# Performance work log

Hardware: AMD Instinct MI355X
Metric: run time of the kernel (lower is better)

## Reference

```python
import jax, jax.numpy as jnp
import numpy as np

SIZE = (128, 128, 128)


def _base_grid():
    # (3, D, H, W): channel i holds the index along spatial dim i (ij meshgrid)
    vs = [jnp.arange(s, dtype=jnp.float32) for s in SIZE]
    return jnp.stack(jnp.meshgrid(*vs, indexing='ij'))


def _grid_sample_3d(vol, grid):
    """torch.nn.functional.grid_sample 3D, mode='bilinear' (trilinear),
    padding_mode='border', align_corners=True.
    vol: (B, C, D, H, W); grid: (B, D, H, W, 3) with last dim = (x, y, z)
    mapping to (W, H, D) axes, per torch semantics."""
    B, C, D, H, W = vol.shape
    gx, gy, gz = grid[..., 0], grid[..., 1], grid[..., 2]
    # unnormalize (align_corners=True) and clamp (border padding)
    ix = jnp.clip((gx + 1.0) * 0.5 * (W - 1), 0.0, W - 1)
    iy = jnp.clip((gy + 1.0) * 0.5 * (H - 1), 0.0, H - 1)
    iz = jnp.clip((gz + 1.0) * 0.5 * (D - 1), 0.0, D - 1)
    ix0f, iy0f, iz0f = jnp.floor(ix), jnp.floor(iy), jnp.floor(iz)
    wx, wy, wz = ix - ix0f, iy - iy0f, iz - iz0f  # (B, D, H, W)
    ix0 = ix0f.astype(jnp.int32)
    iy0 = iy0f.astype(jnp.int32)
    iz0 = iz0f.astype(jnp.int32)
    ix1 = jnp.minimum(ix0 + 1, W - 1)
    iy1 = jnp.minimum(iy0 + 1, H - 1)
    iz1 = jnp.minimum(iz0 + 1, D - 1)

    def sample_one(v, z0, z1, y0, y1, x0, x1, wz_, wy_, wx_):
        # v: (C, D, H, W); index arrays: (D, H, W)
        def g(z, y, x):
            return v[:, z, y, x]  # (C, D, H, W)
        wz_, wy_, wx_ = wz_[None], wy_[None], wx_[None]  # broadcast over C
        c000 = g(z0, y0, x0); c001 = g(z0, y0, x1)
        c010 = g(z0, y1, x0); c011 = g(z0, y1, x1)
        c100 = g(z1, y0, x0); c101 = g(z1, y0, x1)
        c110 = g(z1, y1, x0); c111 = g(z1, y1, x1)
        c00 = c000 * (1 - wx_) + c001 * wx_
        c01 = c010 * (1 - wx_) + c011 * wx_
        c10 = c100 * (1 - wx_) + c101 * wx_
        c11 = c110 * (1 - wx_) + c111 * wx_
        c0 = c00 * (1 - wy_) + c01 * wy_
        c1 = c10 * (1 - wy_) + c11 * wy_
        return c0 * (1 - wz_) + c1 * wz_

    return jax.vmap(sample_one)(vol, iz0, iz1, iy0, iy1, ix0, ix1, wz, wy, wx)


def _warp_dvf(dvf_to_warp, dvf_to_apply):
    g = _base_grid()[None] + dvf_to_apply  # (B, 3, D, H, W)
    scale = jnp.array([2.0 / (s - 1) for s in SIZE], dtype=jnp.float32).reshape(1, 3, 1, 1, 1)
    g = g * scale - 1.0  # 2*(g/(size-1) - 0.5)
    g = jnp.transpose(g, (0, 2, 3, 4, 1))  # (B, D, H, W, 3)
    return _grid_sample_3d(dvf_to_warp, g)


def setup_inputs() -> dict:
    key = jax.random.key(0)
    k1, k2 = jax.random.split(key)
    B = 2
    shape = (B, 3) + SIZE
    return {
        'dvf_fwd': jax.random.normal(k1, shape, dtype=jnp.float32),
        'dvf_bwd': jax.random.normal(k2, shape, dtype=jnp.float32),
    }


def reference(dvf_fwd, dvf_bwd):
    dvf_bwd_warped = _warp_dvf(dvf_bwd, dvf_fwd)
    cycle_error_fwd = dvf_fwd + dvf_bwd_warped
    dvf_fwd_warped = _warp_dvf(dvf_fwd, dvf_bwd)
    cycle_error_bwd = dvf_bwd + dvf_fwd_warped
    return jnp.mean(cycle_error_fwd ** 2) + jnp.mean(cycle_error_bwd ** 2)
```

## Files before the change

kernel.cpp:

```cpp
#include <hip/hip_runtime.h>


#define CS    2097152
#define BS    (3*CS)
#define NTHR  256
#define NBLK_MAIN 8192
#define INV_N (1.0f/12582912.0f)

#if defined(__has_builtin)
#if __has_builtin(__builtin_amdgcn_cvt_pk_fp8_f32) && __has_builtin(__builtin_amdgcn_cvt_pk_f32_fp8)
#define HW_FP8 1
#endif
#endif

typedef float v2f __attribute__((ext_vector_type(2)));
struct __attribute__((aligned(8))) U4 { unsigned x, y, z, w; };

__device__ __forceinline__ unsigned enc1_sw(float x) {
    union { float f; unsigned u; } v; v.f = x;
    unsigned s = v.u >> 31;
    float ax = fminf(fabsf(x), 448.0f);
    if (ax < 0.015625f) return s << 7;
    v.f = ax;
    unsigned u = v.u;
    u += 0x7FFFF + ((u >> 20) & 1);
    unsigned e = (u >> 23) - 120;
    if (e > 15) { e = 15; u = 0x7u << 20; }
    return (s << 7) | (e << 3) | ((u >> 20) & 7);
}
__device__ __forceinline__ float dec1_sw(unsigned b) {
    unsigned s = b >> 7, e = (b >> 3) & 15, m = b & 7;
    union { unsigned u; float f; } v;
    if (e == 0) { float r = (float)m * 0.001953125f; return s ? -r : r; }
    v.u = (s << 31) | ((e + 120) << 23) | (m << 20);
    return v.f;
}
template <bool HI>
__device__ __forceinline__ unsigned enc_pk(float a, float b, unsigned old) {
#ifdef HW_FP8
    return (unsigned)__builtin_amdgcn_cvt_pk_fp8_f32(a, b, (int)old, HI);
#else
    unsigned p = enc1_sw(a) | (enc1_sw(b) << 8);
    return HI ? ((old & 0x0000FFFFu) | (p << 16)) : ((old & 0xFFFF0000u) | p);
#endif
}
template <bool HI>
__device__ __forceinline__ v2f dec_pk(unsigned u) {
#ifdef HW_FP8
    return __builtin_amdgcn_cvt_pk_f32_fp8((int)u, HI);
#else
    unsigned p = HI ? (u >> 16) : u;
    v2f r; r.x = dec1_sw(p & 255); r.y = dec1_sw((p >> 8) & 255);
    return r;
#endif
}
__device__ __forceinline__ uint2 enc_entry(float c0, float c1, float c2,
                                           float p0, float p1, float p2) {
    unsigned lo = enc_pk<false>(c0, c1, 0);
    lo = enc_pk<true>(c2, p0, lo);
    unsigned hi = enc_pk<false>(p1, p2, 0);
    return make_uint2(lo, hi);
}

__global__ __launch_bounds__(NTHR)
void repack_fp8(const float* __restrict__ F, const float* __restrict__ G,
                uint2* __restrict__ PF, uint2* __restrict__ PG) {
    unsigned g = blockIdx.x * NTHR + threadIdx.x;
    int field = g >> 20;
    int b = (g >> 19) & 1;
    unsigned q = g & 0x7FFFF;
    int x = (q & 31) << 2;
    int y = (q >> 5) & 127;
    int z = q >> 12;
    int y1 = min(y + 1, 127);
    const float* src = (field ? G : F) + b * BS;
    uint2* dst = (field ? PG : PF) + b * CS;
    int i0 = (z << 14) + (y << 7) + x;
    int i1 = (z << 14) + (y1 << 7) + x;
    float4 A  = *(const float4*)(src + i0);
    float4 Bc = *(const float4*)(src + CS + i0);
    float4 Cc = *(const float4*)(src + 2 * CS + i0);
    float4 Ap = *(const float4*)(src + i1);
    float4 Bp = *(const float4*)(src + CS + i1);
    float4 Cp = *(const float4*)(src + 2 * CS + i1);
    uint2 e0 = enc_entry(A.x, Bc.x, Cc.x, Ap.x, Bp.x, Cp.x);
    uint2 e1 = enc_entry(A.y, Bc.y, Cc.y, Ap.y, Bp.y, Cp.y);
    uint2 e2 = enc_entry(A.z, Bc.z, Cc.z, Ap.z, Bp.z, Cp.z);
    uint2 e3 = enc_entry(A.w, Bc.w, Cc.w, Ap.w, Bp.w, Cp.w);
    U4 o0; o0.x = e0.x; o0.y = e0.y; o0.z = e1.x; o0.w = e1.y;
    U4 o1; o1.x = e2.x; o1.y = e2.y; o1.z = e3.x; o1.w = e3.y;
    *(U4*)(dst + i0) = o0;
    *(U4*)(dst + i0 + 2) = o1;
}

__global__ __launch_bounds__(NTHR, 8)
void icl_main(const uint2* __restrict__ PF, const uint2* __restrict__ PG,
              const float* __restrict__ F, const float* __restrict__ G,
              float* __restrict__ partial) {
    __shared__ float sA[3072];

    int orig = blockIdx.x;
    int xcd = orig & 7;
    int s = orig >> 3;
    int u = s & 63, tile = s >> 6;
    int ht = ((tile & 7) << 3) | (u & 7);
    int wt = ((tile >> 3) << 3) | (u >> 3);
    int dt = xcd & 1, b = (xcd >> 1) & 1, dir = xcd >> 2;

    const float* Ab = (dir ? G : F) + b * BS;
    const uint2* Vb = (dir ? PF : PG) + b * CS;
    int d0 = dt << 6, h0 = ht << 1, w0 = wt << 3;

    int t = threadIdx.x;
    #pragma unroll
    for (int j = 0; j < 3; ++j) {
        int rem = t << 2;
        int d_l = rem >> 4, h_l = (rem >> 3) & 1, w_l = rem & 7;
        const float4 v = *(const float4*)(Ab + j * CS + ((d0 + d_l) << 14)
                                          + ((h0 + h_l) << 7) + w0 + w_l);
        int Rb = (j * 2 + h_l) * 8 + w_l;
        sA[((Rb + 0) << 6) | ((d_l + Rb + 0) & 63)] = v.x;
        sA[((Rb + 1) << 6) | ((d_l + Rb + 1) & 63)] = v.y;
        sA[((Rb + 2) << 6) | ((d_l + Rb + 2) & 63)] = v.z;
        sA[((Rb + 3) << 6) | ((d_l + Rb + 3) & 63)] = v.w;
    }
    __syncthreads();

    int lane = t & 63, wv = t >> 6;
    int h_l = wv & 1, wseg = wv >> 1;
    int d = d0 + lane, h = h0 + h_l;

    float A0[4], A1[4], A2[4], WX[4], WY[4], WZ[4];
    int AD0[4], AD1[4];
    #pragma unroll
    for (int i = 0; i < 4; ++i) {
        int w_l = (wseg << 2) | i;
        int w = w0 + w_l;
        int R0 = h_l * 8 + w_l, R1 = 16 + R0, R2 = 32 + R0;
        float a0 = sA[(R0 << 6) | ((lane + R0) & 63)];
        float a1 = sA[(R1 << 6) | ((lane + R1) & 63)];
        float a2 = sA[(R2 << 6) | ((lane + R2) & 63)];
        float fx = fminf(fmaxf((float)d + a0, 0.0f), 127.0f);
        float fy = fminf(fmaxf((float)h + a1, 0.0f), 127.0f);
        float fz = fminf(fmaxf((float)w + a2, 0.0f), 127.0f);
        int x0 = (int)fx, y0 = (int)fy, z0 = (int)fz;
        int x0c = min(x0, 126);
        int z1 = min(z0 + 1, 127);
        A0[i] = a0; A1[i] = a1; A2[i] = a2;
        WX[i] = fx - (float)x0c;
        WY[i] = fy - (float)y0;
        WZ[i] = fz - (float)z0;
        AD0[i] = (((z0 << 7) | y0) << 7) + x0c;
        AD1[i] = (((z1 << 7) | y0) << 7) + x0c;
    }
    U4 QA[4], QB[4];
    #pragma unroll
    for (int i = 0; i < 4; ++i) QA[i] = *(const U4*)(Vb + AD0[i]);
    #pragma unroll
    for (int i = 0; i < 4; ++i) QB[i] = *(const U4*)(Vb + AD1[i]);

    float acc = 0.0f;
    #pragma unroll
    for (int i = 0; i < 4; ++i) {
        float wxp = WX[i], wy = WY[i], wz = WZ[i];
        U4 qa = QA[i], qb = QB[i];
        v2f a_lo = dec_pk<false>(qa.x), b_lo = dec_pk<false>(qa.z);
        v2f c_lo = dec_pk<false>(qb.x), d_lo = dec_pk<false>(qb.z);
        float t0 = a_lo.x + wxp * (b_lo.x - a_lo.x);
        float t1 = a_lo.y + wxp * (b_lo.y - a_lo.y);
        float s0 = c_lo.x + wxp * (d_lo.x - c_lo.x);
        float s1 = c_lo.y + wxp * (d_lo.y - c_lo.y);
        float u0 = t0 + wz * (s0 - t0);
        float u1 = t1 + wz * (s1 - t1);
        v2f a_hi = dec_pk<true>(qa.x), b_hi = dec_pk<true>(qa.z);
        v2f c_hi = dec_pk<true>(qb.x), d_hi = dec_pk<true>(qb.z);
        float t2 = a_hi.x + wxp * (b_hi.x - a_hi.x);
        float t3 = a_hi.y + wxp * (b_hi.y - a_hi.y);
        float s2 = c_hi.x + wxp * (d_hi.x - c_hi.x);
        float s3 = c_hi.y + wxp * (d_hi.y - c_hi.y);
        float u2 = t2 + wz * (s2 - t2);
        float u3 = t3 + wz * (s3 - t3);
        v2f a2_ = dec_pk<false>(qa.y), b2_ = dec_pk<false>(qa.w);
        v2f c2_ = dec_pk<false>(qb.y), d2_ = dec_pk<false>(qb.w);
        float t4 = a2_.x + wxp * (b2_.x - a2_.x);
        float t5 = a2_.y + wxp * (b2_.y - a2_.y);
        float s4 = c2_.x + wxp * (d2_.x - c2_.x);
        float s5 = c2_.y + wxp * (d2_.y - c2_.y);
        float u4 = t4 + wz * (s4 - t4);
        float u5 = t5 + wz * (s5 - t5);
        float e0 = A0[i] + (u0 + wy * (u3 - u0));
        float e1 = A1[i] + (u1 + wy * (u4 - u1));
        float e2 = A2[i] + (u2 + wy * (u5 - u2));
        acc += e0 * e0 + e1 * e1 + e2 * e2;
    }

    #pragma unroll
    for (int o = 32; o > 0; o >>= 1) acc += __shfl_down(acc, o);
    __shared__ float ws[NTHR / 64];
    if ((t & 63) == 0) ws[t >> 6] = acc;
    __syncthreads();
    if (t == 0) {
        float ssum = 0.0f;
        #pragma unroll
        for (int i = 0; i < NTHR / 64; ++i) ssum += ws[i];
        partial[orig] = ssum;
    }
}

__device__ __forceinline__ float tri_fb(const float* __restrict__ v,
                                        int zy00, int zy01, int zy10, int zy11,
                                        int x0, int x1,
                                        float wz, float wy, float wx) {
    float c000 = v[zy00 + x0], c001 = v[zy00 + x1];
    float c010 = v[zy01 + x0], c011 = v[zy01 + x1];
    float c100 = v[zy10 + x0], c101 = v[zy10 + x1];
    float c110 = v[zy11 + x0], c111 = v[zy11 + x1];
    float c00 = c000 + wx * (c001 - c000);
    float c01 = c010 + wx * (c011 - c010);
    float c10 = c100 + wx * (c101 - c100);
    float c11 = c110 + wx * (c111 - c110);
    float c0  = c00  + wy * (c01  - c00);
    float c1  = c10  + wy * (c11  - c10);
    return c0 + wz * (c1 - c0);
}

__global__ __launch_bounds__(NTHR, 6)
void icl_partial_fb(const float* __restrict__ F, const float* __restrict__ G,
                    float* __restrict__ partial) {
    __shared__ float sA[6144];
    int orig = blockIdx.x;
    int id = ((orig & 7) << 9) | (orig >> 3);
    int wt  = id & 15;
    int ht  = (id >> 4) & 31;
    int dt  = (id >> 9) & 1;
    int b   = (id >> 10) & 1;
    int dir = id >> 11;
    const float* Ab = (dir ? G : F) + b * BS;
    const float* Vb = (dir ? F : G) + b * BS;
    int d0 = dt << 6, h0 = ht << 2, w0 = wt << 3;
    int t = threadIdx.x;
    #pragma unroll
    for (int j = 0; j < 6; ++j) {
        int L   = (j << 10) + (t << 2);
        int c   = L >> 11;
        int rem = L & 2047;
        int row = rem >> 3;
        int w_l = rem & 7;
        int d_l = row >> 2, h_l = row & 3;
        const float4 v = *(const float4*)(Ab + c * CS + ((d0 + d_l) << 14)
                                          + ((h0 + h_l) << 7) + w0 + w_l);
        int Rb = (c * 4 + h_l) * 8 + w_l;
        sA[((Rb + 0) << 6) | ((d_l + Rb + 0) & 63)] = v.x;
        sA[((Rb + 1) << 6) | ((d_l + Rb + 1) & 63)] = v.y;
        sA[((Rb + 2) << 6) | ((d_l + Rb + 2) & 63)] = v.z;
        sA[((Rb + 3) << 6) | ((d_l + Rb + 3) & 63)] = v.w;
    }
    __syncthreads();
    int lane = t & 63, wv = t >> 6;
    int d = d0 + lane;
    float acc = 0.0f;
    #pragma unroll 4
    for (int i = 0; i < 8; ++i) {
        int h = h0 + wv, w = w0 + i;
        int R0 = (0 * 4 + wv) * 8 + i;
        int R1 = (1 * 4 + wv) * 8 + i;
        int R2 = (2 * 4 + wv) * 8 + i;
        float a0 = sA[(R0 << 6) | ((lane + R0) & 63)];
        float a1 = sA[(R1 << 6) | ((lane + R1) & 63)];
        float a2 = sA[(R2 << 6) | ((lane + R2) & 63)];
        float fx = fminf(fmaxf((float)d + a0, 0.0f), 127.0f);
        float fy = fminf(fmaxf((float)h + a1, 0.0f), 127.0f);
        float fz = fminf(fmaxf((float)w + a2, 0.0f), 127.0f);
        int x0 = (int)fx, y0 = (int)fy, z0 = (int)fz;
        float wx = fx - (float)x0, wy = fy - (float)y0, wz = fz - (float)z0;
        int x1 = min(x0 + 1, 127), y1 = min(y0 + 1, 127), z1 = min(z0 + 1, 127);
        int zy00 = ((z0 << 7) | y0) << 7;
        int zy01 = ((z0 << 7) | y1) << 7;
        int zy10 = ((z1 << 7) | y0) << 7;
        int zy11 = ((z1 << 7) | y1) << 7;
        float s0 = tri_fb(Vb,        zy00, zy01, zy10, zy11, x0, x1, wz, wy, wx);
        float s1 = tri_fb(Vb + CS,   zy00, zy01, zy10, zy11, x0, x1, wz, wy, wx);
        float s2 = tri_fb(Vb + 2*CS, zy00, zy01, zy10, zy11, x0, x1, wz, wy, wx);
        float e0 = a0 + s0, e1 = a1 + s1, e2 = a2 + s2;
        acc += e0 * e0 + e1 * e1 + e2 * e2;
    }
    #pragma unroll
    for (int o = 32; o > 0; o >>= 1) acc += __shfl_down(acc, o);
    __shared__ float ws[NTHR / 64];
    if ((t & 63) == 0) ws[t >> 6] = acc;
    __syncthreads();
    if (t == 0) {
        float s = 0.0f;
        #pragma unroll
        for (int i = 0; i < NTHR / 64; ++i) s += ws[i];
        partial[orig] = s;
    }
}

__global__ __launch_bounds__(NTHR)
void icl_final(const float* __restrict__ partial, float* __restrict__ out, int n) {
    float a = 0.0f;
    for (int i = threadIdx.x; i < n; i += NTHR) a += partial[i];
    #pragma unroll
    for (int o = 32; o > 0; o >>= 1) a += __shfl_down(a, o);
    __shared__ float ws[NTHR / 64];
    if ((threadIdx.x & 63) == 0) ws[threadIdx.x >> 6] = a;
    __syncthreads();
    if (threadIdx.x == 0) {
        float s = 0.0f;
        #pragma unroll
        for (int i = 0; i < NTHR / 64; ++i) s += ws[i];
        out[0] = s * INV_N;
    }
}

extern "C" void kernel_launch(void* const* d_in, const int* in_sizes, int n_in,
                              void* d_out, int out_size, void* d_ws, size_t ws_size,
                              hipStream_t stream) {
    const float* F = (const float*)d_in[0];
    const float* G = (const float*)d_in[1];
    size_t field_bytes = (size_t)2 * CS * sizeof(uint2);
    size_t need = 2 * field_bytes + NBLK_MAIN * sizeof(float) + 256;
    if (ws_size >= need) {
        uint2* PF = (uint2*)d_ws;
        uint2* PG = PF + (size_t)2 * CS;
        float* partial = (float*)(PG + (size_t)2 * CS);
        repack_fp8<<<8192, NTHR, 0, stream>>>(F, G, PF, PG);
        icl_main<<<NBLK_MAIN, NTHR, 0, stream>>>(PF, PG, F, G, partial);
        icl_final<<<1, NTHR, 0, stream>>>(partial, (float*)d_out, NBLK_MAIN);
    } else {
        float* partial = (float*)d_ws;
        icl_partial_fb<<<4096, NTHR, 0, stream>>>(F, G, partial);
        icl_final<<<1, NTHR, 0, stream>>>(partial, (float*)d_out, 4096);
    }
}
```

Measured before the change: 88.08 us.

## Pack full 2x2 y/z corner stencil per voxel into 12-byte fp8 entries

```diff
diff --git a/kernel.cpp b/kernel.cpp
--- a/kernel.cpp
+++ b/kernel.cpp
@@ -5,6 +5,7 @@
 #define BS    (3*CS)
 #define NTHR  256
 #define NBLK_MAIN 8192
+#define EB    12
 #define INV_N (1.0f/12582912.0f)
 
 #if defined(__has_builtin)
@@ -14,7 +15,8 @@
 #endif
 
 typedef float v2f __attribute__((ext_vector_type(2)));
-struct __attribute__((aligned(8))) U4 { unsigned x, y, z, w; };
+struct __attribute__((aligned(4))) U4a4 { unsigned x, y, z, w; };
+struct __attribute__((aligned(4))) U2a4 { unsigned x, y; };
 
 __device__ __forceinline__ unsigned enc1_sw(float x) {
     union { float f; unsigned u; } v; v.f = x;
@@ -54,47 +56,60 @@
     return r;
 #endif
 }
-__device__ __forceinline__ uint2 enc_entry(float c0, float c1, float c2,
-                                           float p0, float p1, float p2) {
-    unsigned lo = enc_pk<false>(c0, c1, 0);
-    lo = enc_pk<true>(c2, p0, lo);
-    unsigned hi = enc_pk<false>(p1, p2, 0);
-    return make_uint2(lo, hi);
-}
 
 __global__ __launch_bounds__(NTHR)
-void repack_fp8(const float* __restrict__ F, const float* __restrict__ G,
-                uint2* __restrict__ PF, uint2* __restrict__ PG) {
+void repack_zp(const float* __restrict__ F, const float* __restrict__ G,
+               char* __restrict__ P) {
     unsigned g = blockIdx.x * NTHR + threadIdx.x;
-    int field = g >> 20;
-    int b = (g >> 19) & 1;
-    unsigned q = g & 0x7FFFF;
-    int x = (q & 31) << 2;
-    int y = (q >> 5) & 127;
-    int z = q >> 12;
-    int y1 = min(y + 1, 127);
+    int x = (g & 31) << 2;
+    unsigned r = g >> 5;
+    int y = r & 127;
+    int z = (r >> 7) & 127;
+    int b = (r >> 14) & 1;
+    int field = (r >> 15) & 1;
     const float* src = (field ? G : F) + b * BS;
-    uint2* dst = (field ? PG : PF) + b * CS;
-    int i0 = (z << 14) + (y << 7) + x;
-    int i1 = (z << 14) + (y1 << 7) + x;
-    float4 A  = *(const float4*)(src + i0);
-    float4 Bc = *(const float4*)(src + CS + i0);
-    float4 Cc = *(const float4*)(src + 2 * CS + i0);
-    float4 Ap = *(const float4*)(src + i1);
-    float4 Bp = *(const float4*)(src + CS + i1);
-    float4 Cp = *(const float4*)(src + 2 * CS + i1);
-    uint2 e0 = enc_entry(A.x, Bc.x, Cc.x, Ap.x, Bp.x, Cp.x);
-    uint2 e1 = enc_entry(A.y, Bc.y, Cc.y, Ap.y, Bp.y, Cp.y);
-    uint2 e2 = enc_entry(A.z, Bc.z, Cc.z, Ap.z, Bp.z, Cp.z);
-    uint2 e3 = enc_entry(A.w, Bc.w, Cc.w, Ap.w, Bp.w, Cp.w);
-    U4 o0; o0.x = e0.x; o0.y = e0.y; o0.z = e1.x; o0.w = e1.y;
-    U4 o1; o1.x = e2.x; o1.y = e2.y; o1.z = e3.x; o1.w = e3.y;
-    *(U4*)(dst + i0) = o0;
-    *(U4*)(dst + i0 + 2) = o1;
+    char* dst = P + (size_t)(field * 2 + b) * ((size_t)EB * CS)
+                  + (size_t)((z << 14) + (y << 7) + x) * EB;
+    int y1 = min(y + 1, 127), z1 = min(z + 1, 127);
+    int iA = (z << 14) + (y << 7) + x;
+    int iB = (z << 14) + (y1 << 7) + x;
+    int iC = (z1 << 14) + (y << 7) + x;
+    int iD = (z1 << 14) + (y1 << 7) + x;
+    float4 A0 = *(const float4*)(src + iA);
+    float4 A1 = *(const float4*)(src + CS + iA);
+    float4 A2 = *(const float4*)(src + 2 * CS + iA);
+    float4 B0 = *(const float4*)(src + iB);
+    float4 B1 = *(const float4*)(src + CS + iB);
+    float4 B2 = *(const float4*)(src + 2 * CS + iB);
+    float4 C0 = *(const float4*)(src + iC);
+    float4 C1 = *(const float4*)(src + CS + iC);
+    float4 C2 = *(const float4*)(src + 2 * CS + iC);
+    float4 D0 = *(const float4*)(src + iD);
+    float4 D1 = *(const float4*)(src + CS + iD);
+    float4 D2 = *(const float4*)(src + 2 * CS + iD);
+    const float* pA0 = (const float*)&A0; const float* pA1 = (const float*)&A1;
+    const float* pA2 = (const float*)&A2; const float* pB0 = (const float*)&B0;
+    const float* pB1 = (const float*)&B1; const float* pB2 = (const float*)&B2;
+    const float* pC0 = (const float*)&C0; const float* pC1 = (const float*)&C1;
+    const float* pC2 = (const float*)&C2; const float* pD0 = (const float*)&D0;
+    const float* pD1 = (const float*)&D1; const float* pD2 = (const float*)&D2;
+    unsigned wrd[12];
+    #pragma unroll
+    for (int k = 0; k < 4; ++k) {
+        wrd[3 * k + 0] = enc_pk<true>(pA2[k], pB0[k], enc_pk<false>(pA0[k], pA1[k], 0));
+        wrd[3 * k + 1] = enc_pk<true>(pC0[k], pC1[k], enc_pk<false>(pB1[k], pB2[k], 0));
+        wrd[3 * k + 2] = enc_pk<true>(pD1[k], pD2[k], enc_pk<false>(pC2[k], pD0[k], 0));
+    }
+    U4a4 s0; s0.x = wrd[0]; s0.y = wrd[1]; s0.z = wrd[2]; s0.w = wrd[3];
+    U4a4 s1; s1.x = wrd[4]; s1.y = wrd[5]; s1.z = wrd[6]; s1.w = wrd[7];
+    U4a4 s2; s2.x = wrd[8]; s2.y = wrd[9]; s2.z = wrd[10]; s2.w = wrd[11];
+    *(U4a4*)(dst) = s0;
+    *(U4a4*)(dst + 16) = s1;
+    *(U4a4*)(dst + 32) = s2;
 }
 
 __global__ __launch_bounds__(NTHR, 8)
-void icl_main(const uint2* __restrict__ PF, const uint2* __restrict__ PG,
+void icl_main(const char* __restrict__ P,
               const float* __restrict__ F, const float* __restrict__ G,
               float* __restrict__ partial) {
     __shared__ float sA[3072];
@@ -108,7 +123,7 @@
     int dt = xcd & 1, b = (xcd >> 1) & 1, dir = xcd >> 2;
 
     const float* Ab = (dir ? G : F) + b * BS;
-    const uint2* Vb = (dir ? PF : PG) + b * CS;
+    const char* Vbc = P + (size_t)((dir ? 0 : 2) + b) * ((size_t)EB * CS);
     int d0 = dt << 6, h0 = ht << 1, w0 = wt << 3;
 
     int t = threadIdx.x;
@@ -131,7 +146,7 @@
     int d = d0 + lane, h = h0 + h_l;
 
     float A0[4], A1[4], A2[4], WX[4], WY[4], WZ[4];
-    int AD0[4], AD1[4];
+    int OFF[4];
     #pragma unroll
     for (int i = 0; i < 4; ++i) {
         int w_l = (wseg << 2) | i;
@@ -145,52 +160,43 @@
         float fz = fminf(fmaxf((float)w + a2, 0.0f), 127.0f);
         int x0 = (int)fx, y0 = (int)fy, z0 = (int)fz;
         int x0c = min(x0, 126);
-        int z1 = min(z0 + 1, 127);
         A0[i] = a0; A1[i] = a1; A2[i] = a2;
         WX[i] = fx - (float)x0c;
         WY[i] = fy - (float)y0;
         WZ[i] = fz - (float)z0;
-        AD0[i] = (((z0 << 7) | y0) << 7) + x0c;
-        AD1[i] = (((z1 << 7) | y0) << 7) + x0c;
-    }
-    U4 QA[4], QB[4];
-    #pragma unroll
-    for (int i = 0; i < 4; ++i) QA[i] = *(const U4*)(Vb + AD0[i]);
-    #pragma unroll
-    for (int i = 0; i < 4; ++i) QB[i] = *(const U4*)(Vb + AD1[i]);
+        OFF[i] = ((((z0 << 7) | y0) << 7) + x0c) * EB;
+    }
+    U4a4 QA[4]; U2a4 QB[4];
+    #pragma unroll
+    for (int i = 0; i < 4; ++i) {
+        QA[i] = *(const U4a4*)(Vbc + OFF[i]);
+        QB[i] = *(const U2a4*)(Vbc + OFF[i] + 16);
+    }
 
     float acc = 0.0f;
     #pragma unroll
     for (int i = 0; i < 4; ++i) {
-        float wxp = WX[i], wy = WY[i], wz = WZ[i];
-        U4 qa = QA[i], qb = QB[i];
-        v2f a_lo = dec_pk<false>(qa.x), b_lo = dec_pk<false>(qa.z);
-        v2f c_lo = dec_pk<false>(qb.x), d_lo = dec_pk<false>(qb.z);
-        float t0 = a_lo.x + wxp * (b_lo.x - a_lo.x);
-        float t1 = a_lo.y + wxp * (b_lo.y - a_lo.y);
-        float s0 = c_lo.x + wxp * (d_lo.x - c_lo.x);
-        float s1 = c_lo.y + wxp * (d_lo.y - c_lo.y);
-        float u0 = t0 + wz * (s0 - t0);
-        float u1 = t1 + wz * (s1 - t1);
-        v2f a_hi = dec_pk<true>(qa.x), b_hi = dec_pk<true>(qa.z);
-        v2f c_hi = dec_pk<true>(qb.x), d_hi = dec_pk<true>(qb.z);
-        float t2 = a_hi.x + wxp * (b_hi.x - a_hi.x);
-        float t3 = a_hi.y + wxp * (b_hi.y - a_hi.y);
-        float s2 = c_hi.x + wxp * (d_hi.x - c_hi.x);
-        float s3 = c_hi.y + wxp * (d_hi.y - c_hi.y);
-        float u2 = t2 + wz * (s2 - t2);
-        float u3 = t3 + wz * (s3 - t3);
-        v2f a2_ = dec_pk<false>(qa.y), b2_ = dec_pk<false>(qa.w);
-        v2f c2_ = dec_pk<false>(qb.y), d2_ = dec_pk<false>(qb.w);
-        float t4 = a2_.x + wxp * (b2_.x - a2_.x);
-        float t5 = a2_.y + wxp * (b2_.y - a2_.y);
-        float s4 = c2_.x + wxp * (d2_.x - c2_.x);
-        float s5 = c2_.y + wxp * (d2_.y - c2_.y);
-        float u4 = t4 + wz * (s4 - t4);
-        float u5 = t5 + wz * (s5 - t5);
-        float e0 = A0[i] + (u0 + wy * (u3 - u0));
-        float e1 = A1[i] + (u1 + wy * (u4 - u1));
-        float e2 = A2[i] + (u2 + wy * (u5 - u2));
+        v2f wx2; wx2.x = WX[i]; wx2.y = WX[i];
+        v2f wz2; wz2.x = WZ[i]; wz2.y = WZ[i];
+        float wy = WY[i];
+        v2f p0 = dec_pk<false>(QA[i].x), p1 = dec_pk<true>(QA[i].x);
+        v2f p2 = dec_pk<false>(QA[i].y), p3 = dec_pk<true>(QA[i].y);
+        v2f p4 = dec_pk<false>(QA[i].z), p5 = dec_pk<true>(QA[i].z);
+        v2f q0 = dec_pk<false>(QA[i].w), q1 = dec_pk<true>(QA[i].w);
+        v2f q2 = dec_pk<false>(QB[i].x), q3 = dec_pk<true>(QB[i].x);
+        v2f q4 = dec_pk<false>(QB[i].y), q5 = dec_pk<true>(QB[i].y);
+        v2f X0 = p0 + wx2 * (q0 - p0);
+        v2f X1 = p1 + wx2 * (q1 - p1);
+        v2f X2 = p2 + wx2 * (q2 - p2);
+        v2f X3 = p3 + wx2 * (q3 - p3);
+        v2f X4 = p4 + wx2 * (q4 - p4);
+        v2f X5 = p5 + wx2 * (q5 - p5);
+        v2f Z0 = X0 + wz2 * (X3 - X0);
+        v2f Z1 = X1 + wz2 * (X4 - X1);
+        v2f Z2 = X2 + wz2 * (X5 - X2);
+        float e0 = A0[i] + (Z0.x + wy * (Z1.y - Z0.x));
+        float e1 = A1[i] + (Z0.y + wy * (Z2.x - Z0.y));
+        float e2 = A2[i] + (Z1.x + wy * (Z2.y - Z1.x));
         acc += e0 * e0 + e1 * e1 + e2 * e2;
     }
 
@@ -319,14 +325,13 @@
                               hipStream_t stream) {
     const float* F = (const float*)d_in[0];
     const float* G = (const float*)d_in[1];
-    size_t field_bytes = (size_t)2 * CS * sizeof(uint2);
-    size_t need = 2 * field_bytes + NBLK_MAIN * sizeof(float) + 256;
+    size_t packed_bytes = (size_t)4 * EB * CS;
+    size_t need = packed_bytes + NBLK_MAIN * sizeof(float) + 256;
     if (ws_size >= need) {
-        uint2* PF = (uint2*)d_ws;
-        uint2* PG = PF + (size_t)2 * CS;
-        float* partial = (float*)(PG + (size_t)2 * CS);
-        repack_fp8<<<8192, NTHR, 0, stream>>>(F, G, PF, PG);
-        icl_main<<<NBLK_MAIN, NTHR, 0, stream>>>(PF, PG, F, G, partial);
+        char* P = (char*)d_ws;
+        float* partial = (float*)(P + packed_bytes);
+        repack_zp<<<16384, NTHR, 0, stream>>>(F, G, P);
+        icl_main<<<NBLK_MAIN, NTHR, 0, stream>>>(P, F, G, partial);
         icl_final<<<1, NTHR, 0, stream>>>(partial, (float*)d_out, NBLK_MAIN);
     } else {
         float* partial = (float*)d_ws;
```

New measurement: 130.3 us. +47.9%, slower.
